# Performance work log

Measured on AMD Instinct MI355X. Metric: run time of the kernel, lower is better.

## Reference

```python
import jax, jax.numpy as jnp
import numpy as np
import math

B, S, D, H, DH = 2, 4096, 1024, 16, 64
CHUNK, RNDS, NBUCK, MLP = 128, 2, 64, 4096


def setup_inputs() -> dict:
    key = jax.random.key(0)
    ks = jax.random.split(key, 8)
    return {
        "inputs": jax.random.normal(ks[0], (B, S, D), jnp.float32),
        "ln1_scale": jnp.ones((D,), jnp.float32),
        "ln1_bias": jnp.zeros((D,), jnp.float32),
        "w_qk": jax.random.normal(ks[1], (D, H, DH), jnp.float32) * 0.02,
        "w_v": jax.random.normal(ks[2], (D, H, DH), jnp.float32) * 0.02,
        "w_out": jax.random.normal(ks[3], (H, DH, D), jnp.float32) * 0.02,
        "rotations": jax.random.normal(ks[4], (DH, RNDS, NBUCK // 2), jnp.float32),
        "ln2_scale": jnp.ones((D,), jnp.float32),
        "ln2_bias": jnp.zeros((D,), jnp.float32),
        "w_mlp1": jax.random.normal(ks[5], (D, MLP), jnp.float32) * 0.02,
        "b_mlp1": jnp.zeros((MLP,), jnp.float32),
        "w_mlp2": jax.random.normal(ks[6], (MLP, D), jnp.float32) * 0.02,
        "b_mlp2": jnp.zeros((D,), jnp.float32),
    }


def _layer_norm(x, scale, bias):
    mu = x.mean(-1, keepdims=True)
    var = ((x - mu) ** 2).mean(-1, keepdims=True)
    return (x - mu) / jnp.sqrt(var + 1e-6) * scale + bias


def _attend_one(q, k, v, buckets):
    # q,k,v: [S,DH]; buckets: [S] int. Sort by bucket (stable via position tiebreak),
    # chunk, attend to own chunk + 1 before + 1 after (look_both_side).
    nC = S // CHUNK
    order = jnp.argsort(buckets * S + jnp.arange(S))  # [S]
    undo = jnp.argsort(order)
    sq = q[order].reshape(nC, CHUNK, DH)
    sk = k[order].reshape(nC, CHUNK, DH)
    sv = v[order].reshape(nC, CHUNK, DH)
    st = order.reshape(nC, CHUNK)  # original token positions
    look = lambda x: jnp.concatenate([x, jnp.roll(x, 1, axis=0), jnp.roll(x, -1, axis=0)], axis=1)
    bk, bv = look(sk), look(sv)
    bt = look(st[..., None])[..., 0]
    dots = jnp.einsum('nqd,nkd->nqk', sq, bk) / math.sqrt(DH)
    # self_mask: a token attends to itself only if nothing else is available
    dots = dots - 1e5 * (st[:, :, None] == bt[:, None, :]).astype(dots.dtype)
    slog = jax.nn.logsumexp(dots, axis=-1)           # [nC,CHUNK]
    o = jnp.einsum('nqk,nkd->nqd', jax.nn.softmax(dots, axis=-1), bv)
    return o.reshape(S, DH)[undo], slog.reshape(S)[undo]


def _lsh_attention(qk, v, rotations):
    # qk,v: [B,H,S,DH]; shared-QK Reformer attention; keys are length-normalized.
    xn = qk / (jnp.linalg.norm(qk, axis=-1, keepdims=True) + 1e-6)
    rot = jnp.einsum('bhsd,drm->bhrsm', xn, rotations)          # [B,H,R,S,NBUCK/2]
    buckets = jnp.argmax(jnp.concatenate([rot, -rot], -1), -1)  # [B,H,R,S]
    rep = lambda x: jnp.broadcast_to(x[:, :, None], (B, H, RNDS, S, DH)).reshape(-1, S, DH)
    o, slog = jax.vmap(_attend_one)(rep(qk), rep(xn), rep(v), buckets.reshape(-1, S))
    o = o.reshape(B, H, RNDS, S, DH)
    slog = slog.reshape(B, H, RNDS, S)
    w = jax.nn.softmax(slog, axis=2)  # combine hash rounds by their logsumexp weight
    return (o * w[..., None]).sum(axis=2)  # [B,H,S,DH]


def reference(inputs, ln1_scale, ln1_bias, w_qk, w_v, w_out, rotations,
              ln2_scale, ln2_bias, w_mlp1, b_mlp1, w_mlp2, b_mlp2):
    x = _layer_norm(inputs, ln1_scale, ln1_bias)
    qk = jnp.einsum('bsd,dhe->bhse', x, w_qk)
    v = jnp.einsum('bsd,dhe->bhse', x, w_v)
    att = _lsh_attention(qk, v, rotations)
    x2 = inputs + jnp.einsum('bhse,hed->bsd', att, w_out)
    y = _layer_norm(x2, ln2_scale, ln2_bias)
    y = jax.nn.gelu(y @ w_mlp1 + b_mlp1) @ w_mlp2 + b_mlp2
    return x2 + y
```

## Files before the change

kernel.cpp:

```cpp
#include <hip/hip_runtime.h>
#include <hip/hip_bf16.h>


typedef short short8 __attribute__((ext_vector_type(8)));
typedef float f32x4 __attribute__((ext_vector_type(4)));
typedef unsigned short us4 __attribute__((ext_vector_type(4)));

__device__ __forceinline__ unsigned short f2bf(float f) {
  unsigned u = __builtin_bit_cast(unsigned, f);
  u += 0x7FFFu + ((u >> 16) & 1u);
  return (unsigned short)(u >> 16);
}

__device__ __forceinline__ float bf2f(unsigned short u) {
  return __builtin_bit_cast(float, ((unsigned)u) << 16);
}

__device__ __forceinline__ float gelu_f(float x) {
  float x3 = x * x * x;
  float t = tanhf(0.7978845608028654f * (x + 0.044715f * x3));
  return 0.5f * x * (1.0f + t);
}

__device__ __forceinline__ void load_lds16(const void* g, void* l) {
  __builtin_amdgcn_global_load_lds(
      (const __attribute__((address_space(1))) unsigned int*)g,
      (__attribute__((address_space(3))) unsigned int*)l, 16, 0, 0);
}

__global__ __launch_bounds__(256) void transpose_cast(
    const float* __restrict__ in, unsigned short* __restrict__ out, int R,
    int C) {
  __shared__ float tile[32][33];
  int ctiles = C >> 5;
  int bx = blockIdx.x % ctiles;
  int by = blockIdx.x / ctiles;
  int tx = threadIdx.x & 31;
  int ty = threadIdx.x >> 5;
#pragma unroll
  for (int i = 0; i < 32; i += 8)
    tile[ty + i][tx] = in[(size_t)(by * 32 + ty + i) * C + bx * 32 + tx];
  __syncthreads();
#pragma unroll
  for (int i = 0; i < 32; i += 8)
    out[(size_t)(bx * 32 + ty + i) * R + by * 32 + tx] = f2bf(tile[tx][ty + i]);
}

__global__ __launch_bounds__(256) void ln_bf16(const float* __restrict__ x,
                                               const float* __restrict__ sc,
                                               const float* __restrict__ bi,
                                               unsigned short* __restrict__ y) {
  int row = blockIdx.x, tid = threadIdx.x, lane = tid & 63, wv = tid >> 6;
  const float* xr = x + (size_t)row * 1024;
  float4 v = *(const float4*)(xr + tid * 4);
  float s1 = v.x + v.y + v.z + v.w;
  float s2 = v.x * v.x + v.y * v.y + v.z * v.z + v.w * v.w;
#pragma unroll
  for (int o = 1; o < 64; o <<= 1) {
    s1 += __shfl_xor(s1, o);
    s2 += __shfl_xor(s2, o);
  }
  __shared__ float a1[4], a2[4];
  if (lane == 0) {
    a1[wv] = s1;
    a2[wv] = s2;
  }
  __syncthreads();
  s1 = a1[0] + a1[1] + a1[2] + a1[3];
  s2 = a2[0] + a2[1] + a2[2] + a2[3];
  float mu = s1 * (1.f / 1024.f);
  float var = s2 * (1.f / 1024.f) - mu * mu;
  float rs = rsqrtf(var + 1e-6f);
  int c = tid * 4;
  us4 o4;
  o4.x = f2bf((v.x - mu) * rs * sc[c + 0] + bi[c + 0]);
  o4.y = f2bf((v.y - mu) * rs * sc[c + 1] + bi[c + 1]);
  o4.z = f2bf((v.z - mu) * rs * sc[c + 2] + bi[c + 2]);
  o4.w = f2bf((v.w - mu) * rs * sc[c + 3] + bi[c + 3]);
  *(us4*)(y + (size_t)row * 1024 + c) = o4;
}

#define GBM 128
#define GBN 128
#define GBK 32

template <int EPI>
__global__ __launch_bounds__(256) void gemm_bt(
    const unsigned short* __restrict__ A, const unsigned short* __restrict__ Bt,
    const float* __restrict__ bias, const float* __restrict__ res,
    float* __restrict__ Cf, unsigned short* __restrict__ Cb, int M, int N,
    int K) {
  __shared__ unsigned short sA[4][GBM * GBK];
  __shared__ unsigned short sB[4][GBN * GBK];
  const int nbx = N / GBN;
  const int nwg = gridDim.x;
  const int cpx = nwg >> 3;
  const int bid = blockIdx.x;
  const int swz = (bid & 7) * cpx + (bid >> 3);
  const int bx = swz % nbx;
  const int by = swz / nbx;
  const int tid = threadIdx.x;
  const int lane = tid & 63;
  const int wave = tid >> 6;
  const int wr = wave >> 1, wc = wave & 1;
  const unsigned short* Abase = A + (size_t)(by * GBM) * K;
  const unsigned short* Bbase = Bt + (size_t)(bx * GBN) * K;

  const int srow_l = wave * 32 + (lane >> 2);
  const int sgl = (lane & 3) ^ ((srow_l >> 1) & 3);
  const unsigned short* Ag = Abase + (size_t)srow_l * K + sgl * 8;
  const unsigned short* Bg = Bbase + (size_t)srow_l * K + sgl * 8;
  const int ldsoff = wave * 32 * GBK;
  const int ldsoff2 = ldsoff + 16 * GBK;

  f32x4 acc[4][4];
#pragma unroll
  for (int m = 0; m < 4; ++m)
#pragma unroll
    for (int n = 0; n < 4; ++n) {
      f32x4 z = {0.f, 0.f, 0.f, 0.f};
      acc[m][n] = z;
    }

  const int KT = K / GBK;

#define STAGE(ktile, slot)                                             \
  do {                                                                 \
    const unsigned short* An_ = Ag + (size_t)(ktile)*GBK;              \
    const unsigned short* Bn_ = Bg + (size_t)(ktile)*GBK;              \
    load_lds16(An_, &sA[(slot)][ldsoff]);                              \
    load_lds16(An_ + (size_t)16 * K, &sA[(slot)][ldsoff2]);            \
    load_lds16(Bn_, &sB[(slot)][ldsoff]);                              \
    load_lds16(Bn_ + (size_t)16 * K, &sB[(slot)][ldsoff2]);            \
  } while (0)

  STAGE(0, 0);
  STAGE(1, 1);
  STAGE(2, 2);
  asm volatile("s_waitcnt vmcnt(8)" ::: "memory");
  __builtin_amdgcn_sched_barrier(0);
  __builtin_amdgcn_s_barrier();

  const int l15 = lane & 15;
  const int lhi = lane >> 4;
  const int arowb = wr * 64 + l15;
  const int browb = wc * 64 + l15;
  const int gsw = (lhi ^ ((l15 >> 1) & 3)) * 8;

  for (int kt = 0; kt < KT; ++kt) {
    const int slot = kt & 3;
    short8 af[4], bfv[4];
#pragma unroll
    for (int m = 0; m < 4; ++m)
      af[m] = *(const short8*)&sA[slot][(arowb + m * 16) * GBK + gsw];
#pragma unroll
    for (int n = 0; n < 4; ++n)
      bfv[n] = *(const short8*)&sB[slot][(browb + n * 16) * GBK + gsw];
    if (kt + 3 < KT) STAGE(kt + 3, (kt + 3) & 3);
    __builtin_amdgcn_s_setprio(1);
#pragma unroll
    for (int m = 0; m < 4; ++m)
#pragma unroll
      for (int n = 0; n < 4; ++n)
        acc[m][n] = __builtin_amdgcn_mfma_f32_16x16x32_bf16(af[m], bfv[n],
                                                            acc[m][n], 0, 0, 0);
    __builtin_amdgcn_s_setprio(0);
    if (kt + 3 < KT) {
      asm volatile("s_waitcnt vmcnt(8)" ::: "memory");
    } else if (kt + 2 < KT) {
      asm volatile("s_waitcnt vmcnt(4)" ::: "memory");
    } else if (kt + 1 < KT) {
      asm volatile("s_waitcnt vmcnt(0)" ::: "memory");
    }
    __builtin_amdgcn_sched_barrier(0);
    __builtin_amdgcn_s_barrier();
  }
#undef STAGE

  const int r0 = by * GBM + wr * 64;
  const int c0 = bx * GBN + wc * 64;
#pragma unroll
  for (int m = 0; m < 4; ++m) {
#pragma unroll
    for (int n = 0; n < 4; ++n) {
#pragma unroll
      for (int i = 0; i < 4; ++i) {
        int rr = r0 + m * 16 + ((lane >> 4) << 2) + i;
        int cc = c0 + n * 16 + (lane & 15);
        float vacc = acc[m][n][i];
        if (EPI == 1) {
          float t = vacc + bias[cc];
          Cb[(size_t)rr * N + cc] = f2bf(gelu_f(t));
        } else if (EPI == 2) {
          float t = vacc + res[(size_t)rr * N + cc];
          if (bias != nullptr) t += bias[cc];
          Cf[(size_t)rr * N + cc] = t;
        } else if (EPI == 3) {
          Cf[(size_t)rr * N + cc] = vacc;
          Cb[(size_t)rr * N + cc] = f2bf(vacc);
        } else if (EPI == 4) {
          Cb[(size_t)rr * N + cc] = f2bf(vacc);
        }
      }
    }
  }
}

__global__ __launch_bounds__(256) void bucket_kernel(
    const float* __restrict__ qk, const float* __restrict__ rot,
    unsigned short* __restrict__ knb, int* __restrict__ buckets) {
  __shared__ float rotl[64 * 64];
  __shared__ float xnl[4][64];
  int tid = threadIdx.x, lane = tid & 63, wv = tid >> 6;
  for (int i = tid; i < 4096; i += 256) rotl[i] = rot[i];
  __syncthreads();
  for (int it = 0; it < 8; ++it) {
    int g = (it * 4096 + blockIdx.x) * 4 + wv;
    int bh = g >> 12;
    int s = g & 4095;
    int b = bh >> 4, h = bh & 15;
    size_t rowoff = (size_t)(b * 4096 + s) * 1024 + h * 64;
    float x = qk[rowoff + lane];
    float ss = x * x;
#pragma unroll
    for (int o = 1; o < 64; o <<= 1) ss += __shfl_xor(ss, o);
    float rn = 1.f / (sqrtf(ss) + 1e-6f);
    float xn = x * rn;
    knb[rowoff + lane] = f2bf(xn);
    xnl[wv][lane] = xn;
    __syncthreads();
    int r_ = lane >> 5, m_ = lane & 31;
    float a = 0.f;
#pragma unroll 16
    for (int d = 0; d < 64; ++d) a += xnl[wv][d] * rotl[d * 64 + r_ * 32 + m_];
    float bv;
    int bi;
    if (a >= 0.f) {
      bv = a;
      bi = m_;
    } else {
      bv = -a;
      bi = m_ + 32;
    }
#pragma unroll
    for (int o = 16; o >= 1; o >>= 1) {
      float ov = __shfl_xor(bv, o);
      int oi = __shfl_xor(bi, o);
      if (ov > bv || (ov == bv && oi < bi)) {
        bv = ov;
        bi = oi;
      }
    }
    if (m_ == 0) buckets[((size_t)bh * 2 + r_) * 4096 + s] = bi;
    __syncthreads();
  }
}

#define HSTR 65

__global__ __launch_bounds__(256) void sort_kernel(
    const int* __restrict__ buckets, int* __restrict__ order) {
  __shared__ unsigned int hist[256 * HSTR];
  __shared__ unsigned int bucketStart[64];
  const int bhr = blockIdx.x;
  const int t = threadIdx.x;
  const int* bk = buckets + (size_t)bhr * 4096;

  unsigned int* hrow = &hist[t * HSTR];
#pragma unroll
  for (int b = 0; b < 64; ++b) hrow[b] = 0u;

  int bks[16];
  {
    const int4* bp = (const int4*)(bk + t * 16);
#pragma unroll
    for (int j4 = 0; j4 < 4; ++j4) {
      int4 v = bp[j4];
      bks[j4 * 4 + 0] = v.x;
      bks[j4 * 4 + 1] = v.y;
      bks[j4 * 4 + 2] = v.z;
      bks[j4 * 4 + 3] = v.w;
    }
  }
#pragma unroll
  for (int j = 0; j < 16; ++j) hrow[bks[j]]++;
  __syncthreads();

  if (t < 64) {
    unsigned int acc = 0;
    for (int t2 = 0; t2 < 256; ++t2) {
      unsigned int c = hist[t2 * HSTR + t];
      hist[t2 * HSTR + t] = acc;
      acc += c;
    }
    bucketStart[t] = acc;
  }
  __syncthreads();
  if (t == 0) {
    unsigned int acc = 0;
    for (int b = 0; b < 64; ++b) {
      unsigned int c = bucketStart[b];
      bucketStart[b] = acc;
      acc += c;
    }
  }
  __syncthreads();

  int* op = order + (size_t)bhr * 4096;
#pragma unroll
  for (int j = 0; j < 16; ++j) {
    int b = bks[j];
    unsigned int pos = bucketStart[b] + hrow[b];
    hrow[b]++;
    op[pos] = t * 16 + j;
  }
}

#define KSTR 72
#define PSTR 136

__global__ __launch_bounds__(256, 2) void lsh_attn_mfma(
    const unsigned short* __restrict__ qb, const unsigned short* __restrict__ knb,
    const unsigned short* __restrict__ vb, const int* __restrict__ order,
    unsigned short* __restrict__ ob, float* __restrict__ slog) {
  __shared__ unsigned short Kls[128 * KSTR];
  __shared__ unsigned short Vt[64 * PSTR];
  __shared__ unsigned short Pls[4][32 * PSTR];
  __shared__ int qtokL[128];
  __shared__ int btok[128];

  const int bid = blockIdx.x;
  const int swz = (bid & 7) * 256 + (bid >> 3);
  const int c = swz & 31;
  const int bhr = swz >> 5;
  const int bh = bhr >> 1;
  const int h = bh & 15, b = bh >> 4;
  const int* ord = order + (size_t)bhr * 4096;
  const int tid = threadIdx.x, lane = tid & 63, wv = tid >> 6;
  const int l15 = lane & 15, lhi = lane >> 4;

  if (tid < 128) qtokL[tid] = ord[c * 128 + tid];
  __syncthreads();

  short8 qf[2][2];
#pragma unroll
  for (int mt = 0; mt < 2; ++mt) {
#pragma unroll
    for (int ks = 0; ks < 2; ++ks) {
      int tok = qtokL[wv * 32 + mt * 16 + l15];
      qf[mt][ks] = *(const short8*)(qb + (size_t)(b * 4096 + tok) * 1024 +
                                    h * 64 + ks * 32 + lhi * 8);
    }
  }

  float mrun[2][4], lrun[2][4];
  f32x4 oacc[2][4];
#pragma unroll
  for (int mt = 0; mt < 2; ++mt)
#pragma unroll
    for (int i = 0; i < 4; ++i) {
      mrun[mt][i] = -1e30f;
      lrun[mt][i] = 0.f;
    }
#pragma unroll
  for (int mt = 0; mt < 2; ++mt)
#pragma unroll
    for (int n = 0; n < 4; ++n) {
      f32x4 z = {0.f, 0.f, 0.f, 0.f};
      oacc[mt][n] = z;
    }

  for (int st = 0; st < 3; ++st) {
    int kc = (st == 0) ? c : (st == 1) ? ((c + 31) & 31) : ((c + 1) & 31);
    __syncthreads();
    {
      int row = tid >> 1, half = tid & 1;
      int ktok = ord[kc * 128 + row];
      if (half == 0) btok[row] = ktok;
      size_t rowoff = (size_t)(b * 4096 + ktok) * 1024 + h * 64 + half * 32;
      const short8* kp = (const short8*)(knb + rowoff);
      const short8* vp = (const short8*)(vb + rowoff);
#pragma unroll
      for (int i = 0; i < 4; ++i)
        *(short8*)&Kls[row * KSTR + half * 32 + i * 8] = kp[i];
#pragma unroll
      for (int i = 0; i < 4; ++i) {
        short8 vw = vp[i];
        int d0 = half * 32 + i * 8;
#pragma unroll
        for (int j = 0; j < 8; ++j)
          Vt[(d0 + j) * PSTR + row] = (unsigned short)vw[j];
      }
    }
    __syncthreads();

    f32x4 sacc[2][8];
#pragma unroll
    for (int mt = 0; mt < 2; ++mt)
#pragma unroll
      for (int n = 0; n < 8; ++n) {
        f32x4 z = {0.f, 0.f, 0.f, 0.f};
        sacc[mt][n] = z;
      }
#pragma unroll
    for (int ks = 0; ks < 2; ++ks) {
      short8 kf[8];
#pragma unroll
      for (int n = 0; n < 8; ++n)
        kf[n] = *(const short8*)&Kls[(n * 16 + l15) * KSTR + ks * 32 + lhi * 8];
#pragma unroll
      for (int mt = 0; mt < 2; ++mt)
#pragma unroll
        for (int n = 0; n < 8; ++n)
          sacc[mt][n] = __builtin_amdgcn_mfma_f32_16x16x32_bf16(
              qf[mt][ks], kf[n], sacc[mt][n], 0, 0, 0);
    }

    int ktA[8];
#pragma unroll
    for (int n = 0; n < 8; ++n) ktA[n] = btok[n * 16 + l15];
#pragma unroll
    for (int mt = 0; mt < 2; ++mt) {
#pragma unroll
      for (int i = 0; i < 4; ++i) {
        int qrow = wv * 32 + mt * 16 + lhi * 4 + i;
        int qt = qtokL[qrow];
        float sv[8];
        float mx = -1e30f;
#pragma unroll
        for (int n = 0; n < 8; ++n) {
          float s = sacc[mt][n][i] * 0.125f;
          if (ktA[n] == qt) s -= 1e5f;
          sv[n] = s;
          mx = fmaxf(mx, s);
        }
#pragma unroll
        for (int d = 1; d < 16; d <<= 1) mx = fmaxf(mx, __shfl_xor(mx, d));
        float mold = mrun[mt][i];
        float mnew = fmaxf(mold, mx);
        float scl = __expf(mold - mnew);
        lrun[mt][i] *= scl;
#pragma unroll
        for (int n = 0; n < 4; ++n) oacc[mt][n][i] *= scl;
        float ps = 0.f;
#pragma unroll
        for (int n = 0; n < 8; ++n) {
          float p = __expf(sv[n] - mnew);
          ps += p;
          Pls[wv][(mt * 16 + lhi * 4 + i) * PSTR + n * 16 + l15] = f2bf(p);
        }
#pragma unroll
        for (int d = 1; d < 16; d <<= 1) ps += __shfl_xor(ps, d);
        lrun[mt][i] = lrun[mt][i] + ps;
        mrun[mt][i] = mnew;
      }
    }

#pragma unroll
    for (int ks = 0; ks < 4; ++ks) {
      short8 pf[2];
#pragma unroll
      for (int mt = 0; mt < 2; ++mt)
        pf[mt] =
            *(const short8*)&Pls[wv][(mt * 16 + l15) * PSTR + ks * 32 + lhi * 8];
      short8 vfr[4];
#pragma unroll
      for (int n = 0; n < 4; ++n)
        vfr[n] = *(const short8*)&Vt[(n * 16 + l15) * PSTR + ks * 32 + lhi * 8];
#pragma unroll
      for (int mt = 0; mt < 2; ++mt)
#pragma unroll
        for (int n = 0; n < 4; ++n)
          oacc[mt][n] = __builtin_amdgcn_mfma_f32_16x16x32_bf16(
              pf[mt], vfr[n], oacc[mt][n], 0, 0, 0);
    }
  }

#pragma unroll
  for (int mt = 0; mt < 2; ++mt) {
#pragma unroll
    for (int i = 0; i < 4; ++i) {
      int qrow = wv * 32 + mt * 16 + lhi * 4 + i;
      int tok = qtokL[qrow];
      float l = lrun[mt][i];
      float invl = 1.f / l;
      if (l15 == 0) slog[(size_t)bhr * 4096 + tok] = logf(l) + mrun[mt][i];
      unsigned short* orow = ob + ((size_t)bhr * 4096 + tok) * 64;
#pragma unroll
      for (int n = 0; n < 4; ++n)
        orow[n * 16 + l15] = f2bf(oacc[mt][n][i] * invl);
    }
  }
}

__global__ __launch_bounds__(256) void combine_rounds(
    const unsigned short* __restrict__ ob, const float* __restrict__ slog,
    unsigned short* __restrict__ att) {
  int g = blockIdx.x * 4 + (threadIdx.x >> 6);
  int lane = threadIdx.x & 63;
  int h = g & 15;
  int bs = g >> 4;
  int b = bs >> 12;
  int s = bs & 4095;
  size_t base = ((size_t)(b * 16 + h) * 2) * 4096 + s;
  size_t i0 = base;
  size_t i1 = base + 4096;
  float s0 = slog[i0], s1 = slog[i1];
  float mx = fmaxf(s0, s1);
  float e0 = __expf(s0 - mx), e1 = __expf(s1 - mx);
  float w0 = e0 / (e0 + e1);
  float w1 = 1.f - w0;
  float v0 = bf2f(ob[i0 * 64 + lane]);
  float v1 = bf2f(ob[i1 * 64 + lane]);
  att[(size_t)bs * 1024 + h * 64 + lane] = f2bf(w0 * v0 + w1 * v1);
}

extern "C" void kernel_launch(void* const* d_in, const int* in_sizes, int n_in,
                              void* d_out, int out_size, void* d_ws,
                              size_t ws_size, hipStream_t stream) {
  const float* inputs = (const float*)d_in[0];
  const float* ln1s = (const float*)d_in[1];
  const float* ln1b = (const float*)d_in[2];
  const float* wqk = (const float*)d_in[3];
  const float* wv = (const float*)d_in[4];
  const float* wout = (const float*)d_in[5];
  const float* rot = (const float*)d_in[6];
  const float* ln2s = (const float*)d_in[7];
  const float* ln2b = (const float*)d_in[8];
  const float* wm1 = (const float*)d_in[9];
  const float* bm1 = (const float*)d_in[10];
  const float* wm2 = (const float*)d_in[11];
  const float* bm2 = (const float*)d_in[12];

  char* w = (char*)d_ws;
  auto alloc = [&](size_t bytes) {
    char* p = w;
    w += (bytes + 255) & ~(size_t)255;
    return p;
  };
  unsigned short* wqk_bt = (unsigned short*)alloc(1024ull * 1024 * 2);
  unsigned short* wv_bt = (unsigned short*)alloc(1024ull * 1024 * 2);
  unsigned short* wout_bt = (unsigned short*)alloc(1024ull * 1024 * 2);
  unsigned short* wm1_bt = (unsigned short*)alloc(4096ull * 1024 * 2);
  unsigned short* wm2_bt = (unsigned short*)alloc(1024ull * 4096 * 2);
  unsigned short* bufA = (unsigned short*)alloc(8192ull * 1024 * 2);
  float* qkf = (float*)alloc(8192ull * 1024 * 4);
  unsigned short* qb = (unsigned short*)alloc(8192ull * 1024 * 2);
  unsigned short* knb = (unsigned short*)alloc(8192ull * 1024 * 2);
  unsigned short* vb = (unsigned short*)alloc(8192ull * 1024 * 2);
  int* buckets = (int*)alloc(64ull * 4096 * 4);
  int* order = (int*)alloc(64ull * 4096 * 4);
  unsigned short* big =
      (unsigned short*)alloc(8192ull * 4096 * 2);
  float* slogb = (float*)alloc(64ull * 4096 * 4);
  float* x2 = qkf;
  unsigned short* obuf = big;
  unsigned short* h1 = big;

  transpose_cast<<<32 * 32, 256, 0, stream>>>(wqk, wqk_bt, 1024, 1024);
  transpose_cast<<<32 * 32, 256, 0, stream>>>(wv, wv_bt, 1024, 1024);
  transpose_cast<<<32 * 32, 256, 0, stream>>>(wout, wout_bt, 1024, 1024);
  transpose_cast<<<32 * 128, 256, 0, stream>>>(wm1, wm1_bt, 1024, 4096);
  transpose_cast<<<128 * 32, 256, 0, stream>>>(wm2, wm2_bt, 4096, 1024);

  ln_bf16<<<8192, 256, 0, stream>>>(inputs, ln1s, ln1b, bufA);

  gemm_bt<3><<<64 * 8, 256, 0, stream>>>(bufA, wqk_bt, nullptr, nullptr, qkf,
                                         qb, 8192, 1024, 1024);
  gemm_bt<4><<<64 * 8, 256, 0, stream>>>(bufA, wv_bt, nullptr, nullptr, nullptr,
                                         vb, 8192, 1024, 1024);

  bucket_kernel<<<4096, 256, 0, stream>>>(qkf, rot, knb, buckets);
  sort_kernel<<<64, 256, 0, stream>>>(buckets, order);
  lsh_attn_mfma<<<2048, 256, 0, stream>>>(qb, knb, vb, order, obuf, slogb);
  combine_rounds<<<32768, 256, 0, stream>>>(obuf, slogb, bufA);

  gemm_bt<2><<<64 * 8, 256, 0, stream>>>(bufA, wout_bt, nullptr, inputs, x2,
                                         nullptr, 8192, 1024, 1024);
  ln_bf16<<<8192, 256, 0, stream>>>(x2, ln2s, ln2b, bufA);
  gemm_bt<1><<<64 * 32, 256, 0, stream>>>(bufA, wm1_bt, bm1, nullptr, nullptr,
                                          h1, 8192, 4096, 1024);
  gemm_bt<2><<<64 * 8, 256, 0, stream>>>(h1, wm2_bt, bm2, x2, (float*)d_out,
                                         nullptr, 8192, 1024, 4096);
}
```

Baseline: 517.3 us.

## Enlarge GEMM block tiles to 256-row with per-wave 128x64 subtiles

Replaces the 128x128 GEMM kernel with a templated version that uses 256-row tiles and 128- or 256-column tiles. Each wave now computes a 128x64 sub-tile, which raises MFMA work per LDS fragment load and cuts global re-reads of A and B. The BN=256 variant runs 512 threads with a 4-deep LDS ring; the BN=128 variant runs a 3-deep ring with matching vmcnt waits. The N=1024 GEMMs now launch only 256 workgroups, so there are fewer resident waves to hide latency, and the large static LDS footprint limits how many blocks fit per CU.

```diff
diff --git a/kernel.cpp b/kernel.cpp
--- a/kernel.cpp
+++ b/kernel.cpp
@@ -80,19 +80,26 @@
   *(us4*)(y + (size_t)row * 1024 + c) = o4;
 }
 
-#define GBM 128
-#define GBN 128
 #define GBK 32
 
-template <int EPI>
-__global__ __launch_bounds__(256) void gemm_bt(
+template <int BN, int EPI>
+__global__ __launch_bounds__(BN == 256 ? 512 : 256, 2) void gemm_big(
     const unsigned short* __restrict__ A, const unsigned short* __restrict__ Bt,
     const float* __restrict__ bias, const float* __restrict__ res,
     float* __restrict__ Cf, unsigned short* __restrict__ Cb, int M, int N,
     int K) {
-  __shared__ unsigned short sA[4][GBM * GBK];
-  __shared__ unsigned short sB[4][GBN * GBK];
-  const int nbx = N / GBN;
+  constexpr int THREADS = (BN == 256) ? 512 : 256;
+  constexpr int RING = (BN == 256) ? 4 : 3;
+  constexpr int DIST = RING - 1;
+  constexpr int WN = THREADS / 128;
+  constexpr int ROWSTEP = THREADS / 4;
+  constexpr int LA = 256 / ROWSTEP;
+  constexpr int LB = BN / ROWSTEP;
+
+  __shared__ unsigned short sA[RING][256 * GBK];
+  __shared__ unsigned short sB[RING][BN * GBK];
+
+  const int nbx = N / BN;
   const int nwg = gridDim.x;
   const int cpx = nwg >> 3;
   const int bid = blockIdx.x;
@@ -101,21 +108,22 @@
   const int by = swz / nbx;
   const int tid = threadIdx.x;
   const int lane = tid & 63;
-  const int wave = tid >> 6;
-  const int wr = wave >> 1, wc = wave & 1;
-  const unsigned short* Abase = A + (size_t)(by * GBM) * K;
-  const unsigned short* Bbase = Bt + (size_t)(bx * GBN) * K;
-
-  const int srow_l = wave * 32 + (lane >> 2);
-  const int sgl = (lane & 3) ^ ((srow_l >> 1) & 3);
-  const unsigned short* Ag = Abase + (size_t)srow_l * K + sgl * 8;
-  const unsigned short* Bg = Bbase + (size_t)srow_l * K + sgl * 8;
-  const int ldsoff = wave * 32 * GBK;
-  const int ldsoff2 = ldsoff + 16 * GBK;
-
-  f32x4 acc[4][4];
-#pragma unroll
-  for (int m = 0; m < 4; ++m)
+  const int wid = tid >> 6;
+  const int wr = wid / WN;
+  const int wc = wid % WN;
+  const int l15 = lane & 15;
+  const int lhi = lane >> 4;
+
+  const int srow = tid >> 2;
+  const int sgl = (tid & 3) ^ ((srow >> 1) & 3);
+  const unsigned short* Ag =
+      A + (size_t)(by * 256 + srow) * K + sgl * 8;
+  const unsigned short* Bg =
+      Bt + (size_t)(bx * BN + srow) * K + sgl * 8;
+
+  f32x4 acc[8][4];
+#pragma unroll
+  for (int m = 0; m < 8; ++m)
 #pragma unroll
     for (int n = 0; n < 4; ++n) {
       f32x4 z = {0.f, 0.f, 0.f, 0.f};
@@ -124,69 +132,82 @@
 
   const int KT = K / GBK;
 
-#define STAGE(ktile, slot)                                             \
-  do {                                                                 \
-    const unsigned short* An_ = Ag + (size_t)(ktile)*GBK;              \
-    const unsigned short* Bn_ = Bg + (size_t)(ktile)*GBK;              \
-    load_lds16(An_, &sA[(slot)][ldsoff]);                              \
-    load_lds16(An_ + (size_t)16 * K, &sA[(slot)][ldsoff2]);            \
-    load_lds16(Bn_, &sB[(slot)][ldsoff]);                              \
-    load_lds16(Bn_ + (size_t)16 * K, &sB[(slot)][ldsoff2]);            \
-  } while (0)
-
-  STAGE(0, 0);
-  STAGE(1, 1);
-  STAGE(2, 2);
-  asm volatile("s_waitcnt vmcnt(8)" ::: "memory");
+  auto STAGE = [&](int ktile, int slot) {
+    const unsigned short* As = Ag + (size_t)ktile * GBK;
+    const unsigned short* Bs = Bg + (size_t)ktile * GBK;
+#pragma unroll
+    for (int i = 0; i < LA; ++i)
+      load_lds16(As + (size_t)i * ROWSTEP * K,
+                 (char*)&sA[slot][0] + tid * 16 + i * (THREADS * 16));
+#pragma unroll
+    for (int i = 0; i < LB; ++i)
+      load_lds16(Bs + (size_t)i * ROWSTEP * K,
+                 (char*)&sB[slot][0] + tid * 16 + i * (THREADS * 16));
+  };
+
+#pragma unroll
+  for (int tI = 0; tI < DIST; ++tI) STAGE(tI, tI);
+  if constexpr (BN == 256) {
+    asm volatile("s_waitcnt vmcnt(8)" ::: "memory");
+  } else {
+    asm volatile("s_waitcnt vmcnt(6)" ::: "memory");
+  }
   __builtin_amdgcn_sched_barrier(0);
   __builtin_amdgcn_s_barrier();
 
-  const int l15 = lane & 15;
-  const int lhi = lane >> 4;
-  const int arowb = wr * 64 + l15;
-  const int browb = wc * 64 + l15;
   const int gsw = (lhi ^ ((l15 >> 1) & 3)) * 8;
-
+  const int arow0 = wr * 128;
+  const int brow0 = wc * 64;
+
+  int slot = 0, sslot = DIST;
   for (int kt = 0; kt < KT; ++kt) {
-    const int slot = kt & 3;
-    short8 af[4], bfv[4];
-#pragma unroll
-    for (int m = 0; m < 4; ++m)
-      af[m] = *(const short8*)&sA[slot][(arowb + m * 16) * GBK + gsw];
+    short8 af[8], bfv[4];
+#pragma unroll
+    for (int m = 0; m < 8; ++m)
+      af[m] = *(const short8*)&sA[slot][(arow0 + m * 16 + l15) * GBK + gsw];
 #pragma unroll
     for (int n = 0; n < 4; ++n)
-      bfv[n] = *(const short8*)&sB[slot][(browb + n * 16) * GBK + gsw];
-    if (kt + 3 < KT) STAGE(kt + 3, (kt + 3) & 3);
+      bfv[n] = *(const short8*)&sB[slot][(brow0 + n * 16 + l15) * GBK + gsw];
+    if (kt + DIST < KT) STAGE(kt + DIST, sslot);
     __builtin_amdgcn_s_setprio(1);
 #pragma unroll
-    for (int m = 0; m < 4; ++m)
+    for (int m = 0; m < 8; ++m)
 #pragma unroll
       for (int n = 0; n < 4; ++n)
         acc[m][n] = __builtin_amdgcn_mfma_f32_16x16x32_bf16(af[m], bfv[n],
                                                             acc[m][n], 0, 0, 0);
     __builtin_amdgcn_s_setprio(0);
-    if (kt + 3 < KT) {
-      asm volatile("s_waitcnt vmcnt(8)" ::: "memory");
-    } else if (kt + 2 < KT) {
-      asm volatile("s_waitcnt vmcnt(4)" ::: "memory");
-    } else if (kt + 1 < KT) {
-      asm volatile("s_waitcnt vmcnt(0)" ::: "memory");
+    if constexpr (BN == 256) {
+      if (kt + 3 < KT) {
+        asm volatile("s_waitcnt vmcnt(8)" ::: "memory");
+      } else if (kt + 2 < KT) {
+        asm volatile("s_waitcnt vmcnt(4)" ::: "memory");
+      } else if (kt + 1 < KT) {
+        asm volatile("s_waitcnt vmcnt(0)" ::: "memory");
+      }
+    } else {
+      if (kt + 2 < KT) {
+        asm volatile("s_waitcnt vmcnt(6)" ::: "memory");
+      } else if (kt + 1 < KT) {
+        asm volatile("s_waitcnt vmcnt(0)" ::: "memory");
+      }
     }
     __builtin_amdgcn_sched_barrier(0);
     __builtin_amdgcn_s_barrier();
-  }
-#undef STAGE
-
-  const int r0 = by * GBM + wr * 64;
-  const int c0 = bx * GBN + wc * 64;
-#pragma unroll
-  for (int m = 0; m < 4; ++m) {
+    slot = (slot == RING - 1) ? 0 : slot + 1;
+    sslot = (sslot == RING - 1) ? 0 : sslot + 1;
+  }
+
+  const int r0 = by * 256 + wr * 128;
+  const int c0 = bx * BN + wc * 64;
+#pragma unroll
+  for (int m = 0; m < 8; ++m) {
 #pragma unroll
     for (int n = 0; n < 4; ++n) {
 #pragma unroll
       for (int i = 0; i < 4; ++i) {
-        int rr = r0 + m * 16 + ((lane >> 4) << 2) + i;
-        int cc = c0 + n * 16 + (lane & 15);
+        int rr = r0 + m * 16 + lhi * 4 + i;
+        int cc = c0 + n * 16 + l15;
         float vacc = acc[m][n][i];
         if (EPI == 1) {
           float t = vacc + bias[cc];
@@ -565,21 +586,22 @@
 
   ln_bf16<<<8192, 256, 0, stream>>>(inputs, ln1s, ln1b, bufA);
 
-  gemm_bt<3><<<64 * 8, 256, 0, stream>>>(bufA, wqk_bt, nullptr, nullptr, qkf,
-                                         qb, 8192, 1024, 1024);
-  gemm_bt<4><<<64 * 8, 256, 0, stream>>>(bufA, wv_bt, nullptr, nullptr, nullptr,
-                                         vb, 8192, 1024, 1024);
+  gemm_big<128, 3><<<32 * 8, 256, 0, stream>>>(bufA, wqk_bt, nullptr, nullptr,
+                                               qkf, qb, 8192, 1024, 1024);
+  gemm_big<128, 4><<<32 * 8, 256, 0, stream>>>(bufA, wv_bt, nullptr, nullptr,
+                                               nullptr, vb, 8192, 1024, 1024);
 
   bucket_kernel<<<4096, 256, 0, stream>>>(qkf, rot, knb, buckets);
   sort_kernel<<<64, 256, 0, stream>>>(buckets, order);
   lsh_attn_mfma<<<2048, 256, 0, stream>>>(qb, knb, vb, order, obuf, slogb);
   combine_rounds<<<32768, 256, 0, stream>>>(obuf, slogb, bufA);
 
-  gemm_bt<2><<<64 * 8, 256, 0, stream>>>(bufA, wout_bt, nullptr, inputs, x2,
-                                         nullptr, 8192, 1024, 1024);
+  gemm_big<128, 2><<<32 * 8, 256, 0, stream>>>(bufA, wout_bt, nullptr, inputs,
+                                               x2, nullptr, 8192, 1024, 1024);
   ln_bf16<<<8192, 256, 0, stream>>>(x2, ln2s, ln2b, bufA);
-  gemm_bt<1><<<64 * 32, 256, 0, stream>>>(bufA, wm1_bt, bm1, nullptr, nullptr,
-                                          h1, 8192, 4096, 1024);
-  gemm_bt<2><<<64 * 8, 256, 0, stream>>>(h1, wm2_bt, bm2, x2, (float*)d_out,
-                                         nullptr, 8192, 1024, 4096);
-}
+  gemm_big<256, 1><<<32 * 16, 512, 0, stream>>>(bufA, wm1_bt, bm1, nullptr,
+                                                nullptr, h1, 8192, 4096, 1024);
+  gemm_big<128, 2><<<32 * 8, 256, 0, stream>>>(h1, wm2_bt, bm2, x2,
+                                               (float*)d_out, nullptr, 8192,
+                                               1024, 4096);
+}
```

Result: slower. 534.7 us (+3.4%).
